# Kernel tuning notes

Measured on AMD Instinct MI355X. Metric: run time of the kernel, lower is better.

Reference implementation:

```python
import jax, jax.numpy as jnp
import numpy as np

K = 20
EPS = 1e-5
NEG_SLOPE = 0.2


def _knn_idx(x, k):
    # x: (B, N, C). Torch: pd = -||xi||^2 + 2 xi.xj - ||xj||^2, topk largest = nearest.
    inner = jnp.einsum('bnc,bmc->bnm', x, x)
    xx = jnp.sum(x * x, axis=-1)  # (B, N)
    pd = 2.0 * inner - xx[:, :, None] - xx[:, None, :]
    _, idx = jax.lax.top_k(pd, k)  # (B, N, k)
    return idx


def _bn_lrelu(h, gamma, beta, axes):
    mean = jnp.mean(h, axis=axes)
    var = jnp.var(h, axis=axes)  # biased, as in torch BN training normalization
    hn = (h - mean) * jax.lax.rsqrt(var + EPS) * gamma + beta
    return jnp.where(hn >= 0, hn, NEG_SLOPE * hn)


def _edge_conv(x, W, gamma, beta, k):
    # x: (B, N, C); W: (O, 2C). Returns (B, N, O).
    idx = _knn_idx(x, k)
    nbr = jax.vmap(lambda xb, ib: xb[ib])(x, idx)  # (B, N, k, C) gather
    center = jnp.broadcast_to(x[:, :, None, :], nbr.shape)
    edge = jnp.concatenate([nbr - center, center], axis=-1)  # (B, N, k, 2C)
    h = jnp.einsum('bnkc,oc->bnko', edge, W)
    h = _bn_lrelu(h, gamma, beta, axes=(0, 1, 2))
    return jnp.max(h, axis=2)  # max over k -> (B, N, O)


def setup_inputs() -> dict:
    key = jax.random.key(0)
    ks = jax.random.split(key, 16)
    B, N = 32, 1024
    d = {'x': jax.random.normal(ks[0], (B, N, 3), dtype=jnp.float32)}
    dims = [(64, 6), (64, 128), (128, 128), (256, 256), (1024, 512)]
    for i, (o, c) in enumerate(dims, start=1):
        d[f'W{i}'] = jax.random.normal(ks[i], (o, c), dtype=jnp.float32) * 0.05
        d[f'g{i}'] = jnp.ones((o,), dtype=jnp.float32)
        d[f'b{i}'] = jnp.zeros((o,), dtype=jnp.float32)
    return d


def reference(x, W1, g1, b1, W2, g2, b2, W3, g3, b3, W4, g4, b4, W5, g5, b5):
    B = x.shape[0]
    x1 = _edge_conv(x, W1, g1, b1, K)    # (B, N, 64)
    x2 = _edge_conv(x1, W2, g2, b2, K)   # (B, N, 64)
    x3 = _edge_conv(x2, W3, g3, b3, K)   # (B, N, 128)
    x4 = _edge_conv(x3, W4, g4, b4, K)   # (B, N, 256)
    cat = jnp.concatenate([x1, x2, x3, x4], axis=-1)  # (B, N, 512)
    h = jnp.einsum('bnc,oc->bno', cat, W5)            # (B, N, 1024)
    h = _bn_lrelu(h, g5, b5, axes=(0, 1))
    out = jnp.max(h, axis=1)  # adaptive max pool over points -> (B, 1024)
    return out.reshape(B, 1, -1)
```

## Files before the change

kernel.cpp:

```cpp
#include <hip/hip_runtime.h>
#include <math.h>

#define BB 32
#define NN 1024
#define KNNK 20
#define PTS (BB*NN)

typedef __attribute__((ext_vector_type(8)))  short short8;
typedef __attribute__((ext_vector_type(4)))  float f32x4;
typedef __attribute__((ext_vector_type(16))) float f32x16;

__device__ __forceinline__ float lrelu(float v){ return v >= 0.f ? v : 0.2f*v; }

__device__ __forceinline__ unsigned short f2b(float x){
    union { float f; unsigned u; } c; c.f = x;
    unsigned r = c.u + 0x7FFFu + ((c.u >> 16) & 1u);
    return (unsigned short)(r >> 16);
}

__global__ void sq_kernel(const float* __restrict__ x, int stride, int C, float* __restrict__ xx){
    int pn = blockIdx.x*256 + threadIdx.x;
    if (pn >= PTS) return;
    const float* r = x + (size_t)pn*stride;
    float s = 0.f;
    for (int c = 0; c < C; ++c){ float v = r[c]; s = fmaf(v, v, s); }
    xx[pn] = s;
}

template<int C>
__global__ void __launch_bounds__(256) dist_kernel(const float* __restrict__ x, int stride,
                                                   const float* __restrict__ xx,
                                                   float* __restrict__ D, int b0){
    constexpr int KC = (C < 32 ? C : 32);
    __shared__ float As[KC][132];
    __shared__ float Bs[KC][132];
    const int tid = threadIdx.x;
    int t = blockIdx.x, ti = 0;
    while (t >= 8 - ti){ t -= 8 - ti; ++ti; }
    const int tj = ti + t;
    const int i0 = ti*128, j0 = tj*128;
    const int bl = blockIdx.z;
    const int b  = b0 + bl;
    const float* xb = x + (size_t)b*NN*stride;
    const int rt = tid >> 4, ct = tid & 15;
    float acc[8][8] = {{0.f}};

    for (int kc = 0; kc < C; kc += KC){
        __syncthreads();
        if constexpr (KC % 4 == 0){
            for (int i = tid; i < 128*(KC/4); i += 256){
                int kq = i % (KC/4), rr = i / (KC/4);
                float4 va = *(const float4*)&xb[(size_t)(i0+rr)*stride + kc + kq*4];
                As[kq*4+0][rr]=va.x; As[kq*4+1][rr]=va.y; As[kq*4+2][rr]=va.z; As[kq*4+3][rr]=va.w;
                float4 vb = *(const float4*)&xb[(size_t)(j0+rr)*stride + kc + kq*4];
                Bs[kq*4+0][rr]=vb.x; Bs[kq*4+1][rr]=vb.y; Bs[kq*4+2][rr]=vb.z; Bs[kq*4+3][rr]=vb.w;
            }
        } else {
            for (int i = tid; i < 128*KC; i += 256){
                int k = i % KC, rr = i / KC;
                As[k][rr] = xb[(size_t)(i0+rr)*stride + kc + k];
                Bs[k][rr] = xb[(size_t)(j0+rr)*stride + kc + k];
            }
        }
        __syncthreads();
        #pragma unroll
        for (int k = 0; k < KC; ++k){
            float4 a0 = *(const float4*)&As[k][rt*8];
            float4 a1 = *(const float4*)&As[k][rt*8+4];
            float4 b0v= *(const float4*)&Bs[k][ct*8];
            float4 b1v= *(const float4*)&Bs[k][ct*8+4];
            float av[8]={a0.x,a0.y,a0.z,a0.w,a1.x,a1.y,a1.z,a1.w};
            float bw[8]={b0v.x,b0v.y,b0v.z,b0v.w,b1v.x,b1v.y,b1v.z,b1v.w};
            #pragma unroll
            for (int i = 0; i < 8; ++i)
                #pragma unroll
                for (int j = 0; j < 8; ++j)
                    acc[i][j] = fmaf(av[i], bw[j], acc[i][j]);
        }
    }
    const float* xxb = xx + b*NN;
    float xi[8], xj[8];
    #pragma unroll
    for (int i=0;i<8;++i) xi[i] = xxb[i0 + rt*8 + i];
    #pragma unroll
    for (int j=0;j<8;++j) xj[j] = xxb[j0 + ct*8 + j];
    #pragma unroll
    for (int i=0;i<8;++i){
        float4 d0, d1;
        d0.x = 2.f*acc[i][0] - xi[i] - xj[0];
        d0.y = 2.f*acc[i][1] - xi[i] - xj[1];
        d0.z = 2.f*acc[i][2] - xi[i] - xj[2];
        d0.w = 2.f*acc[i][3] - xi[i] - xj[3];
        d1.x = 2.f*acc[i][4] - xi[i] - xj[4];
        d1.y = 2.f*acc[i][5] - xi[i] - xj[5];
        d1.z = 2.f*acc[i][6] - xi[i] - xj[6];
        d1.w = 2.f*acc[i][7] - xi[i] - xj[7];
        float* drow = &D[((size_t)bl*NN + i0 + rt*8 + i)*NN + j0 + ct*8];
        *(float4*)drow = d0;
        *(float4*)(drow+4) = d1;
    }
    if (ti != tj){
        #pragma unroll
        for (int j=0;j<8;++j){
            float4 m0, m1;
            m0.x = 2.f*acc[0][j] - xj[j] - xi[0];
            m0.y = 2.f*acc[1][j] - xj[j] - xi[1];
            m0.z = 2.f*acc[2][j] - xj[j] - xi[2];
            m0.w = 2.f*acc[3][j] - xj[j] - xi[3];
            m1.x = 2.f*acc[4][j] - xj[j] - xi[4];
            m1.y = 2.f*acc[5][j] - xj[j] - xi[5];
            m1.z = 2.f*acc[6][j] - xj[j] - xi[6];
            m1.w = 2.f*acc[7][j] - xj[j] - xi[7];
            float* mrow = &D[((size_t)bl*NN + j0 + ct*8 + j)*NN + i0 + rt*8];
            *(float4*)mrow = m0;
            *(float4*)(mrow+4) = m1;
        }
    }
}

__global__ void __launch_bounds__(256) topk_kernel(const float* __restrict__ D,
                                                   int* __restrict__ idxout, int baseRow){
    const int tid = threadIdx.x;
    const int wv = tid >> 6, lane = tid & 63;
    const int rid = blockIdx.x*4 + wv;
    const float* drow = D + (size_t)rid * NN;
    float v[16];
    #pragma unroll
    for (int i2 = 0; i2 < 16; ++i2) v[i2] = drow[i2*64 + lane];
    int* orow = idxout + ((size_t)baseRow + rid) * KNNK;
    for (int t = 0; t < KNNK; ++t){
        float bv = v[0]; int bs = 0;
        #pragma unroll
        for (int i2 = 1; i2 < 16; ++i2){ if (v[i2] > bv){ bv = v[i2]; bs = i2; } }
        int bj = bs*64 + lane;
        #pragma unroll
        for (int m = 32; m; m >>= 1){
            float ov = __shfl_xor(bv, m);
            int   oj = __shfl_xor(bj, m);
            if (ov > bv || (ov == bv && oj < bj)){ bv = ov; bj = oj; }
        }
        int clr = ((bj & 63) == lane) ? (bj >> 6) : -1;
        #pragma unroll
        for (int i2 = 0; i2 < 16; ++i2) if (i2 == clr) v[i2] = -INFINITY;
        if (lane == 0) orow[t] = bj;
    }
}

template<int C, int O>
__global__ void __launch_bounds__(256) gemmG_kernel(const float* __restrict__ x, int stride,
                                                    const float* __restrict__ W,
                                                    float* __restrict__ G1, float* __restrict__ Gd){
    constexpr int KC = (C < 32 ? C : 32);
    __shared__ float Xl [KC][68];
    __shared__ float W1l[KC][68];
    __shared__ float W2l[KC][68];
    const int tid = threadIdx.x;
    const int r0 = blockIdx.x * 64;
    const int o0 = blockIdx.y * 64;
    const int rt = tid & 15, ct = tid >> 4;

    float a1[4][4] = {{0.f}}, a2[4][4] = {{0.f}};
    for (int kc = 0; kc < C; kc += KC){
        __syncthreads();
        for (int i = tid; i < KC*64; i += 256){
            int k = i % KC, rr = i / KC;
            Xl [k][rr] = x[(size_t)(r0+rr)*stride + kc + k];
            W1l[k][rr] = W[(size_t)(o0+rr)*(2*C) + kc + k];
            W2l[k][rr] = W[(size_t)(o0+rr)*(2*C) + C + kc + k];
        }
        __syncthreads();
        #pragma unroll
        for (int k = 0; k < KC; ++k){
            float4 xa = *(const float4*)&Xl [k][rt*4];
            float4 w1 = *(const float4*)&W1l[k][ct*4];
            float4 w2 = *(const float4*)&W2l[k][ct*4];
            float xv[4] = {xa.x, xa.y, xa.z, xa.w};
            #pragma unroll
            for (int i = 0; i < 4; ++i){
                a1[i][0] = fmaf(xv[i], w1.x, a1[i][0]);
                a1[i][1] = fmaf(xv[i], w1.y, a1[i][1]);
                a1[i][2] = fmaf(xv[i], w1.z, a1[i][2]);
                a1[i][3] = fmaf(xv[i], w1.w, a1[i][3]);
                a2[i][0] = fmaf(xv[i], w2.x, a2[i][0]);
                a2[i][1] = fmaf(xv[i], w2.y, a2[i][1]);
                a2[i][2] = fmaf(xv[i], w2.z, a2[i][2]);
                a2[i][3] = fmaf(xv[i], w2.w, a2[i][3]);
            }
        }
    }
    #pragma unroll
    for (int i = 0; i < 4; ++i){
        size_t row = (size_t)(r0 + rt*4 + i);
        float4 g1v = make_float4(a1[i][0], a1[i][1], a1[i][2], a1[i][3]);
        float4 gdv = make_float4(a2[i][0]-a1[i][0], a2[i][1]-a1[i][1],
                                 a2[i][2]-a1[i][2], a2[i][3]-a1[i][3]);
        *(float4*)&G1[row*O + o0 + ct*4] = g1v;
        *(float4*)&Gd[row*O + o0 + ct*4] = gdv;
    }
}

template<int O>
__global__ void __launch_bounds__(256) gather_kernel(const float* __restrict__ G1,
                                                     const float* __restrict__ Gd,
                                                     const int* __restrict__ idxg, int bgbase,
                                                     float* __restrict__ catslice,
                                                     float* __restrict__ stats){
    constexpr int PP = 256 / O;
    constexpr int NP = 16;
    __shared__ int nbs[NP][KNNK];
    const int tid = threadIdx.x;
    const int p0 = blockIdx.x * NP;
    for (int i = tid; i < NP*KNNK; i += 256){
        int pp = i / KNNK, kk = i - pp*KNNK;
        int pl = p0 + pp;
        int nb = idxg[(size_t)(bgbase + pl)*KNNK + kk];
        nbs[pp][kk] = ((pl >> 10) << 10) + nb;
    }
    __syncthreads();
    const int o  = tid % O;
    const int pq = tid / O;
    float s1 = 0.f, s2 = 0.f;
    for (int pp = pq; pp < NP; pp += PP){
        int pl = p0 + pp;
        float d = Gd[(size_t)pl*O + o];
        float mx = -INFINITY, ls = 0.f, lq = 0.f;
        #pragma unroll
        for (int kk = 0; kk < KNNK; ++kk){
            float g = G1[(size_t)nbs[pp][kk]*O + o];
            mx = fmaxf(mx, g);
            ls += g;
            lq = fmaf(g, g, lq);
        }
        s1 += ls + 20.f*d;
        s2 += lq + 2.f*d*ls + 20.f*d*d;
        catslice[(size_t)(bgbase + pl)*512 + o] = mx + d;
    }
    int rep = blockIdx.x & 63;
    atomicAdd(&stats[rep*2*O + o],     s1);
    atomicAdd(&stats[rep*2*O + O + o], s2);
}

__global__ void fin_kernel(const float* __restrict__ stats, int O, float cnt,
                           float* __restrict__ mean, float* __restrict__ invstd){
    int o = threadIdx.x;
    if (o >= O) return;
    float s1 = 0.f, s2 = 0.f;
    for (int r = 0; r < 64; ++r){
        s1 += stats[r*2*O + o];
        s2 += stats[r*2*O + O + o];
    }
    float m = s1 / cnt;
    float v = s2 / cnt - m*m;
    mean[o] = m;
    invstd[o] = rsqrtf(v + 1e-5f);
}

template<int O>
__global__ void apply_kernel(float* __restrict__ catslice,
                             const float* __restrict__ mean, const float* __restrict__ invstd,
                             const float* __restrict__ g, const float* __restrict__ bt){
    int i = blockIdx.x*256 + threadIdx.x;
    int pn = i / O, o = i - pn*O;
    float* p = &catslice[(size_t)pn*512 + o];
    float hn = (*p - mean[o]) * invstd[o] * g[o] + bt[o];
    *p = lrelu(hn);
}

__global__ void tob16_kernel(const float* __restrict__ src, unsigned short* __restrict__ dst, int n4){
    int i = blockIdx.x*256 + threadIdx.x;
    if (i >= n4) return;
    float4 v = *(const float4*)&src[(size_t)i*4];
    ushort4 o;
    o.x = f2b(v.x); o.y = f2b(v.y); o.z = f2b(v.z); o.w = f2b(v.w);
    *(ushort4*)&dst[(size_t)i*4] = o;
}

__global__ void __launch_bounds__(256) l5m_kernel(const unsigned short* __restrict__ Am,
                                                  const unsigned short* __restrict__ Bm,
                                                  float* __restrict__ pmax,
                                                  float* __restrict__ psum,
                                                  float* __restrict__ psq){
    __shared__ __align__(16) unsigned short As[128][64];
    __shared__ __align__(16) unsigned short Bs[128][64];
    const int tid = threadIdx.x;
    const int r0 = blockIdx.x * 128;
    const int o0 = blockIdx.y * 128;
    const int w = tid >> 6, lane = tid & 63;
    const int m32 = lane & 31, kh = lane >> 5;
    const int wm = (w & 1) * 64;
    const int wn = (w >> 1) * 64;

    f32x16 acc[2][2];
    #pragma unroll
    for (int i=0;i<2;++i)
        #pragma unroll
        for (int j=0;j<2;++j)
            #pragma unroll
            for (int r=0;r<16;++r) acc[i][j][r] = 0.f;

    for (int kc = 0; kc < 512; kc += 64){
        __syncthreads();
        #pragma unroll
        for (int t = 0; t < 4; ++t){
            int i = tid + t*256;
            int rr = i >> 3, ch = i & 7;
            int sl = ch ^ (rr & 7);
            *(uint4*)&As[rr][sl*8] = *(const uint4*)&Am[(size_t)(r0+rr)*512 + kc + ch*8];
            *(uint4*)&Bs[rr][sl*8] = *(const uint4*)&Bm[(size_t)(o0+rr)*512 + kc + ch*8];
        }
        __syncthreads();
        #pragma unroll
        for (int q = 0; q < 4; ++q){
            int lk = q*2 + kh;
            short8 a[2], bfr[2];
            #pragma unroll
            for (int mb = 0; mb < 2; ++mb){
                int rA = wm + mb*32 + m32;
                a[mb] = *(const short8*)&As[rA][(lk ^ (rA & 7))*8];
            }
            #pragma unroll
            for (int nb = 0; nb < 2; ++nb){
                int rB = wn + nb*32 + m32;
                bfr[nb] = *(const short8*)&Bs[rB][(lk ^ (rB & 7))*8];
            }
            #pragma unroll
            for (int mb = 0; mb < 2; ++mb)
                #pragma unroll
                for (int nb = 0; nb < 2; ++nb)
                    acc[mb][nb] = __builtin_amdgcn_mfma_f32_32x32x16_bf16(a[mb], bfr[nb], acc[mb][nb], 0, 0, 0);
        }
    }
    __syncthreads();
    float* red = (float*)&As[0][0];
    #pragma unroll
    for (int nb = 0; nb < 2; ++nb){
        float mx = -INFINITY, s1 = 0.f, s2 = 0.f;
        #pragma unroll
        for (int mb = 0; mb < 2; ++mb)
            #pragma unroll
            for (int r = 0; r < 16; ++r){
                float v = acc[mb][nb][r];
                mx = fmaxf(mx, v); s1 += v; s2 = fmaf(v, v, s2);
            }
        mx = fmaxf(mx, __shfl_xor(mx, 32));
        s1 += __shfl_xor(s1, 32);
        s2 += __shfl_xor(s2, 32);
        if (lane < 32){
            int col = wn + nb*32 + m32;
            float* p = red + ((size_t)(w & 1) * 128 + col) * 3;
            p[0] = mx; p[1] = s1; p[2] = s2;
        }
    }
    __syncthreads();
    if (tid < 128){
        const float* p0 = red + (size_t)tid*3;
        const float* p1 = red + (size_t)(128 + tid)*3;
        float mx = fmaxf(p0[0], p1[0]);
        float s1 = p0[1] + p1[1];
        float s2 = p0[2] + p1[2];
        size_t pi = (size_t)blockIdx.x*1024 + o0 + tid;
        pmax[pi] = mx; psum[pi] = s1; psq[pi] = s2;
    }
}

__global__ void fin5_kernel(const float* __restrict__ pmax, const float* __restrict__ psum,
                            const float* __restrict__ psq,
                            const float* __restrict__ g, const float* __restrict__ bt,
                            float* __restrict__ out){
    int o = blockIdx.x*256 + threadIdx.x;
    float s1 = 0.f, s2 = 0.f;
    for (int r = 0; r < 256; ++r){
        s1 += psum[(size_t)r*1024 + o];
        s2 += psq [(size_t)r*1024 + o];
    }
    float m  = s1 / 32768.f;
    float v  = s2 / 32768.f - m*m;
    float is = rsqrtf(v + 1e-5f);
    float gg = g[o], bb2 = bt[o];
    for (int b = 0; b < 32; ++b){
        float mx = -INFINITY;
        #pragma unroll
        for (int ns = 0; ns < 8; ++ns) mx = fmaxf(mx, pmax[((size_t)b*8 + ns)*1024 + o]);
        float hn = (mx - m) * is * gg + bb2;
        out[(size_t)b*1024 + o] = lrelu(hn);
    }
}

extern "C" void kernel_launch(void* const* d_in, const int* in_sizes, int n_in,
                              void* d_out, int out_size, void* d_ws, size_t ws_size,
                              hipStream_t stream) {
    (void)in_sizes; (void)n_in; (void)out_size;
    const float* x  = (const float*)d_in[0];
    const float* W1 = (const float*)d_in[1];  const float* g1 = (const float*)d_in[2];  const float* b1 = (const float*)d_in[3];
    const float* W2 = (const float*)d_in[4];  const float* g2 = (const float*)d_in[5];  const float* b2 = (const float*)d_in[6];
    const float* W3 = (const float*)d_in[7];  const float* g3 = (const float*)d_in[8];  const float* b3 = (const float*)d_in[9];
    const float* W4 = (const float*)d_in[10]; const float* g4 = (const float*)d_in[11]; const float* b4 = (const float*)d_in[12];
    const float* W5 = (const float*)d_in[13]; const float* g5 = (const float*)d_in[14]; const float* b5 = (const float*)d_in[15];
    float* out = (float*)d_out;

    const size_t fixedBytes = (size_t)PTS*512*4 + (size_t)PTS*KNNK*4 + (size_t)PTS*4
                            + (size_t)64*2*256*4 + 2048*4 + 3*(size_t)256*1024*4
                            + (size_t)1024*512*2;
    int CB;
    if      (ws_size >= fixedBytes + (size_t)32*NN*NN*4) CB = 32;
    else if (ws_size >= fixedBytes + (size_t)16*NN*NN*4) CB = 16;
    else                                                 CB = 8;
    const size_t Rbytes = (size_t)CB*NN*NN*4;

    char* wsp = (char*)d_ws;
    float* cat    = (float*)wsp; wsp += (size_t)PTS*512*4;
    char*  R      = wsp;         wsp += Rbytes;
    int*   idx    = (int*)  wsp; wsp += (size_t)PTS*KNNK*4;
    float* xx     = (float*)wsp; wsp += (size_t)PTS*4;
    float* stats  = (float*)wsp; wsp += (size_t)64*2*256*4;
    float* mean   = (float*)wsp; wsp += 1024*4;
    float* invstd = (float*)wsp; wsp += 1024*4;
    float* pmax   = (float*)wsp; wsp += (size_t)256*1024*4;
    float* psum   = (float*)wsp; wsp += (size_t)256*1024*4;
    float* psq    = (float*)wsp; wsp += (size_t)256*1024*4;
    unsigned short* W5b = (unsigned short*)wsp; wsp += (size_t)1024*512*2;

    float* Dbuf  = (float*)R;
    float* G1    = (float*)R;
    float* GdS   = (float*)(R + (size_t)16*1024*1024);
    float* GdB   = (float*)(R + (size_t)32*1024*1024);
    unsigned short* catB = (unsigned short*)R;

    const float cntE = (float)(PTS*KNNK);
    const int nch = 32 / CB;
    const bool bigG = (Rbytes >= (size_t)64*1024*1024);

    sq_kernel<<<PTS/256, 256, 0, stream>>>(x, 3, 3, xx);
    for (int bc = 0; bc < nch; ++bc){
        dist_kernel<3><<<dim3(36,1,CB), 256, 0, stream>>>(x, 3, xx, Dbuf, bc*CB);
        topk_kernel<<<CB*1024/4, 256, 0, stream>>>(Dbuf, idx, bc*CB*1024);
    }
    hipMemsetAsync(stats, 0, 64*2*256*4, stream);
    gemmG_kernel<3,64><<<dim3(512,1), 256, 0, stream>>>(x, 3, W1, G1, GdS);
    gather_kernel<64><<<2048, 256, 0, stream>>>(G1, GdS, idx, 0, cat + 0, stats);
    fin_kernel<<<1, 64, 0, stream>>>(stats, 64, cntE, mean, invstd);
    apply_kernel<64><<<PTS*64/256, 256, 0, stream>>>(cat + 0, mean, invstd, g1, b1);

    sq_kernel<<<PTS/256, 256, 0, stream>>>(cat + 0, 512, 64, xx);
    for (int bc = 0; bc < nch; ++bc){
        dist_kernel<64><<<dim3(36,1,CB), 256, 0, stream>>>(cat + 0, 512, xx, Dbuf, bc*CB);
        topk_kernel<<<CB*1024/4, 256, 0, stream>>>(Dbuf, idx, bc*CB*1024);
    }
    hipMemsetAsync(stats, 0, 64*2*256*4, stream);
    gemmG_kernel<64,64><<<dim3(512,1), 256, 0, stream>>>(cat + 0, 512, W2, G1, GdS);
    gather_kernel<64><<<2048, 256, 0, stream>>>(G1, GdS, idx, 0, cat + 64, stats);
    fin_kernel<<<1, 64, 0, stream>>>(stats, 64, cntE, mean, invstd);
    apply_kernel<64><<<PTS*64/256, 256, 0, stream>>>(cat + 64, mean, invstd, g2, b2);

    sq_kernel<<<PTS/256, 256, 0, stream>>>(cat + 64, 512, 64, xx);
    for (int bc = 0; bc < nch; ++bc){
        dist_kernel<64><<<dim3(36,1,CB), 256, 0, stream>>>(cat + 64, 512, xx, Dbuf, bc*CB);
        topk_kernel<<<CB*1024/4, 256, 0, stream>>>(Dbuf, idx, bc*CB*1024);
    }
    hipMemsetAsync(stats, 0, 64*2*256*4, stream);
    gemmG_kernel<64,128><<<dim3(512,2), 256, 0, stream>>>(cat + 64, 512, W3, G1, GdS);
    gather_kernel<128><<<2048, 256, 0, stream>>>(G1, GdS, idx, 0, cat + 128, stats);
    fin_kernel<<<1, 128, 0, stream>>>(stats, 128, cntE, mean, invstd);
    apply_kernel<128><<<PTS*128/256, 256, 0, stream>>>(cat + 128, mean, invstd, g3, b3);

    sq_kernel<<<PTS/256, 256, 0, stream>>>(cat + 128, 512, 128, xx);
    for (int bc = 0; bc < nch; ++bc){
        dist_kernel<128><<<dim3(36,1,CB), 256, 0, stream>>>(cat + 128, 512, xx, Dbuf, bc*CB);
        topk_kernel<<<CB*1024/4, 256, 0, stream>>>(Dbuf, idx, bc*CB*1024);
    }
    hipMemsetAsync(stats, 0, 64*2*256*4, stream);
    if (bigG){
        gemmG_kernel<128,256><<<dim3(512,4), 256, 0, stream>>>(cat + 128, 512, W4, G1, GdB);
        gather_kernel<256><<<2048, 256, 0, stream>>>(G1, GdB, idx, 0, cat + 256, stats);
    } else {
        for (int bg = 0; bg < 4; ++bg){
            gemmG_kernel<128,256><<<dim3(128,4), 256, 0, stream>>>(cat + 128 + (size_t)bg*8192*512, 512, W4, G1, GdS);
            gather_kernel<256><<<512, 256, 0, stream>>>(G1, GdS, idx, bg*8192, cat + 256, stats);
        }
    }
    fin_kernel<<<1, 256, 0, stream>>>(stats, 256, cntE, mean, invstd);
    apply_kernel<256><<<PTS*256/256, 256, 0, stream>>>(cat + 256, mean, invstd, g4, b4);

    tob16_kernel<<<PTS*512/4/256, 256, 0, stream>>>(cat, catB, PTS*512/4);
    tob16_kernel<<<1024*512/4/256, 256, 0, stream>>>(W5, W5b, 1024*512/4);
    l5m_kernel<<<dim3(256, 8), 256, 0, stream>>>(catB, W5b, pmax, psum, psq);
    fin5_kernel<<<4, 256, 0, stream>>>(pmax, psum, psq, g5, b5, out);
}
```

Measured before the change: 1.253 ms.

## Replace iterative top-k argmax with radix-select threshold and vectorize neighbor gather

The top-k kernel now maps distances to order-preserving unsigned keys and finds the 20th-largest value with a 32-step bitwise radix search using wave ballots and popcounts. It then writes every index strictly above that threshold, followed by ties until 20 are filled. This replaces 20 rounds of per-lane max plus shuffle reductions. Output order changes from sorted to index order, and tie-breaking may differ, which only matters if downstream code is order-insensitive. Separately, the gather kernel handles 4 output channels per thread with float4 loads and stores to cut per-element memory instructions.

```diff
diff --git a/kernel.cpp b/kernel.cpp
--- a/kernel.cpp
+++ b/kernel.cpp
@@ -124,25 +124,39 @@
     const int wv = tid >> 6, lane = tid & 63;
     const int rid = blockIdx.x*4 + wv;
     const float* drow = D + (size_t)rid * NN;
-    float v[16];
-    #pragma unroll
-    for (int i2 = 0; i2 < 16; ++i2) v[i2] = drow[i2*64 + lane];
+    unsigned u[16];
+    #pragma unroll
+    for (int i = 0; i < 16; ++i){
+        unsigned bits = __float_as_uint(drow[i*64 + lane]);
+        unsigned m = (bits & 0x80000000u) ? 0xFFFFFFFFu : 0x80000000u;
+        u[i] = bits ^ m;
+    }
+    unsigned t = 0u;
+    for (int b = 31; b >= 0; --b){
+        unsigned cand = t | (1u << b);
+        int cnt = 0;
+        #pragma unroll
+        for (int i = 0; i < 16; ++i)
+            cnt += (int)__popcll(__ballot(u[i] >= cand));
+        if (cnt >= KNNK) t = cand;
+    }
+    const unsigned long long lt = (lane == 0) ? 0ull : ((~0ull) >> (64 - lane));
     int* orow = idxout + ((size_t)baseRow + rid) * KNNK;
-    for (int t = 0; t < KNNK; ++t){
-        float bv = v[0]; int bs = 0;
-        #pragma unroll
-        for (int i2 = 1; i2 < 16; ++i2){ if (v[i2] > bv){ bv = v[i2]; bs = i2; } }
-        int bj = bs*64 + lane;
-        #pragma unroll
-        for (int m = 32; m; m >>= 1){
-            float ov = __shfl_xor(bv, m);
-            int   oj = __shfl_xor(bj, m);
-            if (ov > bv || (ov == bv && oj < bj)){ bv = ov; bj = oj; }
-        }
-        int clr = ((bj & 63) == lane) ? (bj >> 6) : -1;
-        #pragma unroll
-        for (int i2 = 0; i2 < 16; ++i2) if (i2 == clr) v[i2] = -INFINITY;
-        if (lane == 0) orow[t] = bj;
+    int cbase = 0;
+    #pragma unroll
+    for (int i = 0; i < 16; ++i){
+        bool gt2 = (u[i] > t);
+        unsigned long long mask = __ballot(gt2);
+        if (gt2) orow[cbase + (int)__popcll(mask & lt)] = i*64 + lane;
+        cbase += (int)__popcll(mask);
+    }
+    for (int i = 0; i < 16; ++i){
+        if (cbase >= KNNK) break;
+        bool eq = (u[i] == t);
+        unsigned long long mask = __ballot(eq);
+        int pos = cbase + (int)__popcll(mask & lt);
+        if (eq && pos < KNNK) orow[pos] = i*64 + lane;
+        cbase += (int)__popcll(mask);
     }
 }
 
@@ -205,7 +219,8 @@
                                                      const int* __restrict__ idxg, int bgbase,
                                                      float* __restrict__ catslice,
                                                      float* __restrict__ stats){
-    constexpr int PP = 256 / O;
+    constexpr int OG = O/4;
+    constexpr int PP = 256/OG;
     constexpr int NP = 16;
     __shared__ int nbs[NP][KNNK];
     const int tid = threadIdx.x;
@@ -213,31 +228,45 @@
     for (int i = tid; i < NP*KNNK; i += 256){
         int pp = i / KNNK, kk = i - pp*KNNK;
         int pl = p0 + pp;
-        int nb = idxg[(size_t)(bgbase + pl)*KNNK + kk];
-        nbs[pp][kk] = ((pl >> 10) << 10) + nb;
+        nbs[pp][kk] = ((pl >> 10) << 10) + idxg[(size_t)(bgbase + pl)*KNNK + kk];
     }
     __syncthreads();
-    const int o  = tid % O;
-    const int pq = tid / O;
-    float s1 = 0.f, s2 = 0.f;
+    const int o4 = (tid % OG)*4;
+    const int pq = tid / OG;
+    float S1[4] = {0.f,0.f,0.f,0.f}, S2[4] = {0.f,0.f,0.f,0.f};
     for (int pp = pq; pp < NP; pp += PP){
         int pl = p0 + pp;
-        float d = Gd[(size_t)pl*O + o];
-        float mx = -INFINITY, ls = 0.f, lq = 0.f;
+        float4 dv = *(const float4*)&Gd[(size_t)pl*O + o4];
+        float d[4] = {dv.x, dv.y, dv.z, dv.w};
+        float mx[4] = {-INFINITY,-INFINITY,-INFINITY,-INFINITY};
+        float ls[4] = {0.f,0.f,0.f,0.f}, lq[4] = {0.f,0.f,0.f,0.f};
         #pragma unroll
         for (int kk = 0; kk < KNNK; ++kk){
-            float g = G1[(size_t)nbs[pp][kk]*O + o];
-            mx = fmaxf(mx, g);
-            ls += g;
-            lq = fmaf(g, g, lq);
-        }
-        s1 += ls + 20.f*d;
-        s2 += lq + 2.f*d*ls + 20.f*d*d;
-        catslice[(size_t)(bgbase + pl)*512 + o] = mx + d;
+            float4 gv = *(const float4*)&G1[(size_t)nbs[pp][kk]*O + o4];
+            float ga[4] = {gv.x, gv.y, gv.z, gv.w};
+            #pragma unroll
+            for (int c = 0; c < 4; ++c){
+                mx[c] = fmaxf(mx[c], ga[c]);
+                ls[c] += ga[c];
+                lq[c] = fmaf(ga[c], ga[c], lq[c]);
+            }
+        }
+        float4 outv;
+        float* op = &outv.x;
+        #pragma unroll
+        for (int c = 0; c < 4; ++c){
+            S1[c] += ls[c] + 20.f*d[c];
+            S2[c] += lq[c] + 2.f*d[c]*ls[c] + 20.f*d[c]*d[c];
+            op[c] = mx[c] + d[c];
+        }
+        *(float4*)&catslice[(size_t)(bgbase + pl)*512 + o4] = outv;
     }
     int rep = blockIdx.x & 63;
-    atomicAdd(&stats[rep*2*O + o],     s1);
-    atomicAdd(&stats[rep*2*O + O + o], s2);
+    #pragma unroll
+    for (int c = 0; c < 4; ++c){
+        atomicAdd(&stats[rep*2*O + o4 + c],     S1[c]);
+        atomicAdd(&stats[rep*2*O + O + o4 + c], S2[c]);
+    }
 }
 
 __global__ void fin_kernel(const float* __restrict__ stats, int O, float cnt,
```

Result: no change. 1.235 ms (-1.5%).
